# Kernel optimization log

Hardware: AMD Instinct MI355X
Metric: run time of the kernel (lower is better)

Reference implementation:

```python
import jax, jax.numpy as jnp
import numpy as np

N, T, D_MODEL, H, DK = 4, 4096, 1024, 16, 64


def setup_inputs() -> dict:
    key = jax.random.key(0)
    ks = jax.random.split(key, 16)
    randn = lambda k, sh: jax.random.normal(k, sh, dtype=jnp.float32)
    # linear weights stored (in, out) so y = x @ W + b (math-equivalent to torch Linear)
    scale = 1.0 / np.sqrt(D_MODEL)
    return {
        "x_k": randn(ks[0], (N, T, D_MODEL)),
        "x_v": randn(ks[1], (N, T, D_MODEL)),
        "x_q": randn(ks[2], (N, T, D_MODEL)),
        "mask": jnp.ones((N, T), dtype=jnp.int32),
        "Wk": randn(ks[3], (D_MODEL, H * DK)) * scale,
        "bk": randn(ks[4], (H * DK,)) * 0.02,
        "Wv": randn(ks[5], (D_MODEL, H * DK)) * scale,
        "bv": randn(ks[6], (H * DK,)) * 0.02,
        "Wq": randn(ks[7], (D_MODEL, H * DK)) * scale,
        "bq": randn(ks[8], (H * DK,)) * 0.02,
        "alpha_w": randn(ks[9], (DK,)),
        "beta_w": randn(ks[10], (DK,)),
        "Wr": randn(ks[11], (DK, DK)) * (1.0 / np.sqrt(DK)),
        "br": randn(ks[12], (DK,)) * 0.02,
        "Wfc": randn(ks[13], (H * DK, D_MODEL)) * scale,
        "bfc": randn(ks[14], (D_MODEL,)) * 0.02,
    }


def _split_heads(x):  # (n, t, h*d) -> (n, h, t, d)
    n, t, _ = x.shape
    return x.reshape(n, t, H, DK).transpose(0, 2, 1, 3)


def reference(x_k, x_v, x_q, mask, Wk, bk, Wv, bv, Wq, bq,
              alpha_w, beta_w, Wr, br, Wfc, bfc):
    scale = DK ** (-0.5)
    k = _split_heads(x_k @ Wk + bk)  # (n, h, t, d)
    v = _split_heads(x_v @ Wv + bv)
    q = _split_heads(x_q @ Wq + bq)

    m = (mask == 0)[:, None, :]  # (n, 1, t) True where masked
    neg_inf = jnp.finfo(q.dtype).min

    # alpha pooling over queries -> global query (n, h, d)
    alpha = jnp.einsum('nhtd,d->nht', q, alpha_w) * scale
    alpha = jnp.where(m, neg_inf, alpha)
    alpha = jax.nn.softmax(alpha, axis=-1)
    global_query = jnp.einsum('nht,nhtd->nhd', alpha, q)

    # p = broadcast(global_query) * k, then beta pooling -> global key
    p = global_query[:, :, None, :] * k  # (n, h, t, d)
    beta = jnp.einsum('nhtd,d->nht', p, beta_w) * scale
    beta = jnp.where(m, neg_inf, beta)
    beta = jax.nn.softmax(beta, axis=-1)
    global_key = jnp.einsum('nht,nhtd->nhd', beta, p)

    u = global_key[:, :, None, :] * v  # (n, h, t, d)
    u_r = u @ Wr + br
    A = u_r + q  # (n, h, t, d)
    A = A.transpose(0, 2, 1, 3).reshape(N, T, H * DK)
    return A @ Wfc + bfc
```

## Files before the change

### kernel.cpp

```cpp
#include <hip/hip_runtime.h>

typedef __bf16 bf16x8 __attribute__((ext_vector_type(8)));
typedef float f32x4 __attribute__((ext_vector_type(4)));
typedef unsigned int u32x4 __attribute__((ext_vector_type(4)));
typedef unsigned short u16x4 __attribute__((ext_vector_type(4)));
typedef unsigned short u16x8 __attribute__((ext_vector_type(8)));

#define SEQ_T 4096
#define DMODEL 1024
#define HEADS 16
#define DKH 64
#define MTOK 16384

#define AS1 __attribute__((address_space(1)))
#define AS3 __attribute__((address_space(3)))

__device__ __forceinline__ unsigned short f2bf(float f) {
  unsigned u = __builtin_bit_cast(unsigned int, f);
  u += 0x7FFFu + ((u >> 16) & 1u);
  return (unsigned short)(u >> 16);
}
__device__ __forceinline__ float bf2f(unsigned short h) {
  unsigned u = ((unsigned)h) << 16;
  return __builtin_bit_cast(float, u);
}
__device__ __forceinline__ void gload16(const unsigned short* g, unsigned short* l) {
  __builtin_amdgcn_global_load_lds((const AS1 unsigned int*)(g),
                                   (AS3 unsigned int*)(l), 16, 0, 0);
}

__device__ __forceinline__ void cvt_block(const float* __restrict__ x,
                                          unsigned short* __restrict__ y,
                                          size_t b, int tid) {
  f32x4 a[4];
#pragma unroll
  for (int i = 0; i < 4; ++i) a[i] = *(const f32x4*)(x + b + i * 1024 + tid * 4);
#pragma unroll
  for (int i = 0; i < 4; ++i) {
    u16x4 o;
#pragma unroll
    for (int j = 0; j < 4; ++j) o[j] = f2bf(a[i][j]);
    *(u16x4*)(y + b + i * 1024 + tid * 4) = o;
  }
}

__global__ void __launch_bounds__(256) k_cvt(const float* __restrict__ x,
                                             unsigned short* __restrict__ y) {
  cvt_block(x, y, (size_t)blockIdx.x * 4096, threadIdx.x);
}

__global__ void __launch_bounds__(256) k_cvt3(const float* __restrict__ xq,
                                              const float* __restrict__ xk,
                                              const float* __restrict__ xv,
                                              unsigned short* __restrict__ oq,
                                              unsigned short* __restrict__ ok,
                                              unsigned short* __restrict__ ov) {
  const int which = blockIdx.x >> 12;
  const float* x = which == 0 ? xq : (which == 1 ? xk : xv);
  unsigned short* y = which == 0 ? oq : (which == 1 ? ok : ov);
  cvt_block(x, y, (size_t)(blockIdx.x & 4095) * 4096, threadIdx.x);
}

__global__ void __launch_bounds__(256) k_wtrans(const float* __restrict__ W,
                                                unsigned short* __restrict__ Wt,
                                                int K, int N) {
  __shared__ float tile[32][33];
  int bn = blockIdx.x * 32, bk = blockIdx.y * 32;
  int tx = threadIdx.x, ty = threadIdx.y;
#pragma unroll
  for (int j = 0; j < 32; j += 8)
    tile[ty + j][tx] = W[(size_t)(bk + ty + j) * N + bn + tx];
  __syncthreads();
#pragma unroll
  for (int j = 0; j < 32; j += 8)
    Wt[(size_t)(bn + ty + j) * K + bk + tx] = f2bf(tile[tx][ty + j]);
}

#define BM 128
#define BN 128
#define BK 64

template <int OBF, int SCORE, int FUSEA>
__global__ void __launch_bounds__(256, 2)
k_gemm(const unsigned short* __restrict__ A, const unsigned short* __restrict__ Bt,
       const float* __restrict__ bias, void* __restrict__ C,
       const int* __restrict__ mask, const float* __restrict__ swt,
       float* __restrict__ sbuf, const unsigned short* __restrict__ qadd,
       int M, int N, int K) {
  __shared__ unsigned short As[BM * BK];
  __shared__ unsigned short Bs[BN * BK];
  const int tid = threadIdx.x;
  const int lane = tid & 63, wid = tid >> 6;
  const int wr = wid >> 1, wc = wid & 1;
  const int l15 = lane & 15, l4 = lane >> 4;

  const int nwg = gridDim.x * gridDim.y;
  const int flat = blockIdx.x + blockIdx.y * gridDim.x;
  const int rm = (flat & 7) * (nwg >> 3) + (flat >> 3);
  const int bx = rm % gridDim.x, by = rm / gridDim.x;
  const int bm = by * BM, bn = bx * BN;

  const unsigned short* Btn = FUSEA ? Bt + ((size_t)(bm >> 12) << 20) : Bt;
  const float* biasn = FUSEA ? bias + ((bm >> 12) << 10) : bias;

  f32x4 acc[4][4];
#pragma unroll
  for (int i = 0; i < 4; ++i)
#pragma unroll
    for (int j = 0; j < 4; ++j)
#pragma unroll
      for (int e = 0; e < 4; ++e) acc[i][j][e] = 0.f;

  const int sgr = lane >> 3;
  const int sgc = (lane & 7) ^ sgr;

  for (int kt = 0; kt < K; kt += BK) {
    __syncthreads();
#pragma unroll
    for (int j = 0; j < 4; ++j) {
      int rb = wid * 32 + j * 8;
      gload16(A + (size_t)(bm + rb + sgr) * K + kt + sgc * 8, As + rb * BK);
    }
#pragma unroll
    for (int j = 0; j < 4; ++j) {
      int rb = wid * 32 + j * 8;
      gload16(Btn + (size_t)(bn + rb + sgr) * K + kt + sgc * 8, Bs + rb * BK);
    }
    __syncthreads();
#pragma unroll
    for (int kh = 0; kh < 2; ++kh) {
      bf16x8 af[4], bfr[4];
#pragma unroll
      for (int m = 0; m < 4; ++m) {
        int ra = wr * 64 + m * 16 + l15;
        int sl = (kh * 4 + l4) ^ (ra & 7);
        af[m] = *(const bf16x8*)(As + ra * BK + sl * 8);
      }
#pragma unroll
      for (int n = 0; n < 4; ++n) {
        int rb = wc * 64 + n * 16 + l15;
        int sl = (kh * 4 + l4) ^ (rb & 7);
        bfr[n] = *(const bf16x8*)(Bs + rb * BK + sl * 8);
      }
#pragma unroll
      for (int m = 0; m < 4; ++m)
#pragma unroll
        for (int n = 0; n < 4; ++n)
          acc[m][n] = __builtin_amdgcn_mfma_f32_16x16x32_bf16(af[m], bfr[n],
                                                              acc[m][n], 0, 0, 0);
    }
  }

  const int crow = bm + wr * 64 + l4 * 4;
  const int ccol = bn + wc * 64 + l15;

  float pacc[4][4];
  const float* wrow = nullptr;
  if (SCORE == 1) wrow = swt;
  if (SCORE) {
#pragma unroll
    for (int m = 0; m < 4; ++m)
#pragma unroll
      for (int e = 0; e < 4; ++e) pacc[m][e] = 0.f;
  }

#pragma unroll
  for (int m = 0; m < 4; ++m)
#pragma unroll
    for (int n = 0; n < 4; ++n) {
      int c = ccol + n * 16;
      float bj = biasn[c];
      float wg = SCORE ? wrow[n * 16 + l15] : 0.f;
#pragma unroll
      for (int e = 0; e < 4; ++e) {
        int r = crow + m * 16 + e;
        float v = acc[m][n][e] + bj;
        if (FUSEA) v += bf2f(qadd[(size_t)r * N + c]);
        if (SCORE) pacc[m][e] += v * wg;
        if (OBF)
          ((unsigned short*)C)[(size_t)r * N + c] = f2bf(v);
        else
          ((float*)C)[(size_t)r * N + c] = v;
      }
    }

  if (SCORE) {
#pragma unroll
    for (int m = 0; m < 4; ++m)
#pragma unroll
      for (int e = 0; e < 4; ++e) {
        float p = pacc[m][e];
        p += __shfl_xor(p, 1);
        p += __shfl_xor(p, 2);
        p += __shfl_xor(p, 4);
        p += __shfl_xor(p, 8);
        if (l15 == 0) {
          int r = crow + m * 16 + e;
          int t = r & (SEQ_T - 1), n = r >> 12;
          float sc = p * 0.125f;
          if (mask[n * SEQ_T + t] == 0) sc = -3.0e38f;
          sbuf[((size_t)n * HEADS + bx * 2 + wc) * SEQ_T + t] = sc;
        }
      }
  }
}

__global__ void __launch_bounds__(256) k_softmax(const float* __restrict__ s,
                                                 float* __restrict__ mxo,
                                                 float* __restrict__ invo) {
  __shared__ float red[4];
  const int tid = threadIdx.x, lane = tid & 63, wid = tid >> 6;
  const float* sb = s + (size_t)blockIdx.x * SEQ_T;
  float m = -3.4e38f;
  for (int t = tid; t < SEQ_T; t += 256) m = fmaxf(m, sb[t]);
#pragma unroll
  for (int o = 1; o < 64; o <<= 1) m = fmaxf(m, __shfl_xor(m, o));
  if (lane == 0) red[wid] = m;
  __syncthreads();
  m = fmaxf(fmaxf(red[0], red[1]), fmaxf(red[2], red[3]));
  __syncthreads();
  float sum = 0.f;
  for (int t = tid; t < SEQ_T; t += 256) sum += __expf(sb[t] - m);
#pragma unroll
  for (int o = 1; o < 64; o <<= 1) sum += __shfl_xor(sum, o);
  if (lane == 0) red[wid] = sum;
  __syncthreads();
  if (tid == 0) {
    mxo[blockIdx.x] = m;
    invo[blockIdx.x] = 1.f / (red[0] + red[1] + red[2] + red[3]);
  }
}

__global__ void __launch_bounds__(256) k_wsum(const unsigned short* __restrict__ X,
                                              const float* __restrict__ s,
                                              const float* __restrict__ mxv,
                                              const float* __restrict__ invv,
                                              float* __restrict__ pbuf) {
  __shared__ float part[16][64];
  const int nh = blockIdx.x >> 4, chunk = blockIdx.x & 15;
  const int n = nh >> 4, h = nh & 15;
  const int tid = threadIdx.x, lane = tid & 63, wid = tid >> 6;
  const int tsub = lane >> 4, dl = lane & 15;
  const float mx = mxv[nh], inv = invv[nh];
  const float* sb = s + (size_t)nh * SEQ_T + chunk * 256;
  const size_t base = ((size_t)n * SEQ_T + chunk * 256) * DMODEL + h * DKH + dl * 4;
  f32x4 acc = {0.f, 0.f, 0.f, 0.f};
  for (int t = wid * 4 + tsub; t < 256; t += 16) {
    float w = __expf(sb[t] - mx) * inv;
    u16x4 xv = *(const u16x4*)(X + base + (size_t)t * DMODEL);
    acc[0] += w * bf2f(xv[0]);
    acc[1] += w * bf2f(xv[1]);
    acc[2] += w * bf2f(xv[2]);
    acc[3] += w * bf2f(xv[3]);
  }
  int g = wid * 4 + tsub;
#pragma unroll
  for (int e = 0; e < 4; ++e) part[g][dl * 4 + e] = acc[e];
  __syncthreads();
  if (tid < 64) {
    float v = 0.f;
#pragma unroll
    for (int gg = 0; gg < 16; ++gg) v += part[gg][tid];
    pbuf[(size_t)blockIdx.x * 64 + tid] = v;
  }
}

__global__ void __launch_bounds__(256) k_wksb(const float* __restrict__ Wk,
                                              const float* __restrict__ bk,
                                              const float* __restrict__ pbuf,
                                              const float* __restrict__ bw,
                                              float* __restrict__ gq,
                                              unsigned short* __restrict__ WksT,
                                              float* __restrict__ bks) {
  const int nh = blockIdx.x, tid = threadIdx.x;
  const int n = nh >> 4, h = nh & 15;
  __shared__ float wvs[64];
  if (tid < 64) {
    float v = 0.f;
#pragma unroll
    for (int c = 0; c < 16; ++c) v += pbuf[((size_t)nh * 16 + c) * 64 + tid];
    gq[(size_t)nh * 64 + tid] = v;
    wvs[tid] = v * bw[tid];
  }
  __syncthreads();
  int c0 = tid * 4;
  u16x4 o;
#pragma unroll
  for (int i = 0; i < 4; ++i) {
    int c = c0 + i;
    const float* wr = Wk + (size_t)c * DMODEL + h * DKH;
    float acc = 0.f;
#pragma unroll
    for (int dd = 0; dd < 64; dd += 4) {
      f32x4 w4 = *(const f32x4*)(wr + dd);
      acc += w4[0] * wvs[dd] + w4[1] * wvs[dd + 1] + w4[2] * wvs[dd + 2] +
             w4[3] * wvs[dd + 3];
    }
    o[i] = f2bf(acc);
  }
  *(u16x4*)(WksT + (size_t)n * 16 * DMODEL + (size_t)h * DMODEL + c0) = o;
  if (tid < 64) {
    float p = bk[h * 64 + tid] * wvs[tid];
#pragma unroll
    for (int ofs = 1; ofs < 64; ofs <<= 1) p += __shfl_xor(p, ofs);
    if (tid == 0) bks[nh] = p;
  }
}

__global__ void __launch_bounds__(128) k_score(const unsigned short* __restrict__ xk,
                                               const unsigned short* __restrict__ WksT,
                                               const float* __restrict__ bks,
                                               const int* __restrict__ mask,
                                               float* __restrict__ sbuf) {
  __shared__ unsigned short Xs[64 * 32];
  __shared__ unsigned short Ws[16 * 32];
  const int tid = threadIdx.x, lane = tid & 63, wid = tid >> 6;
  const int l15 = lane & 15, l4 = lane >> 4;
  const int bm = blockIdx.x * 64;
  const int n = bm >> 12;
  const unsigned short* Wn = WksT + (size_t)n * 16 * DMODEL;

  f32x4 acc[2];
#pragma unroll
  for (int m = 0; m < 2; ++m)
#pragma unroll
    for (int e = 0; e < 4; ++e) acc[m][e] = 0.f;

  const int srow = lane >> 2, scol = (lane & 3) * 8;
  for (int kt = 0; kt < DMODEL; kt += 32) {
    __syncthreads();
#pragma unroll
    for (int j = 0; j < 2; ++j) {
      int rb = wid * 32 + j * 16;
      gload16(xk + (size_t)(bm + rb + srow) * DMODEL + kt + scol, Xs + rb * 32);
    }
    if (wid == 0) gload16(Wn + (size_t)srow * DMODEL + kt + scol, Ws);
    __syncthreads();
    bf16x8 bfr = *(const bf16x8*)(Ws + l15 * 32 + l4 * 8);
#pragma unroll
    for (int m = 0; m < 2; ++m) {
      bf16x8 af = *(const bf16x8*)(Xs + (wid * 32 + m * 16 + l15) * 32 + l4 * 8);
      acc[m] = __builtin_amdgcn_mfma_f32_16x16x32_bf16(af, bfr, acc[m], 0, 0, 0);
    }
  }
  const int h = l15;
  const float bh = bks[n * 16 + h];
#pragma unroll
  for (int m = 0; m < 2; ++m)
#pragma unroll
    for (int e = 0; e < 4; ++e) {
      int r = bm + wid * 32 + m * 16 + l4 * 4 + e;
      int t = r & (SEQ_T - 1);
      float sc = (acc[m][e] + bh) * 0.125f;
      if (mask[n * SEQ_T + t] == 0) sc = -3.0e38f;
      sbuf[((size_t)n * HEADS + h) * SEQ_T + t] = sc;
    }
}

__global__ void __launch_bounds__(256) k_bwsum(const unsigned short* __restrict__ xk,
                                               const float* __restrict__ s,
                                               const float* __restrict__ smx,
                                               const float* __restrict__ sinv,
                                               float* __restrict__ part) {
  __shared__ float eb[16][64];
  const int tc = blockIdx.x, n = blockIdx.y, tid = threadIdx.x;
#pragma unroll
  for (int i = 0; i < 4; ++i) {
    int idx = i * 256 + tid;
    int h = idx >> 6, t = idx & 63;
    int nh = n * 16 + h;
    eb[h][t] = __expf(s[(size_t)nh * SEQ_T + tc * 64 + t] - smx[nh]) * sinv[nh];
  }
  __syncthreads();
  const int c0 = tid * 4;
  f32x4 acc[16];
#pragma unroll
  for (int h = 0; h < 16; ++h)
#pragma unroll
    for (int e = 0; e < 4; ++e) acc[h][e] = 0.f;
  const unsigned short* xb = xk + ((size_t)n * SEQ_T + tc * 64) * DMODEL + c0;
  for (int t = 0; t < 64; ++t) {
    u16x4 xr = *(const u16x4*)(xb + (size_t)t * DMODEL);
    float x0 = bf2f(xr[0]), x1 = bf2f(xr[1]), x2 = bf2f(xr[2]), x3 = bf2f(xr[3]);
#pragma unroll
    for (int h = 0; h < 16; ++h) {
      float w = eb[h][t];
      acc[h][0] += w * x0;
      acc[h][1] += w * x1;
      acc[h][2] += w * x2;
      acc[h][3] += w * x3;
    }
  }
#pragma unroll
  for (int h = 0; h < 16; ++h)
    *(f32x4*)(part + (((size_t)(n * 64 + tc)) * 16 + h) * DMODEL + c0) = acc[h];
}

__global__ void __launch_bounds__(256) k_gkrw(const float* __restrict__ part,
                                              const unsigned short* __restrict__ WkT,
                                              const float* __restrict__ bk,
                                              const float* __restrict__ gq,
                                              const float* __restrict__ Wr,
                                              const float* __restrict__ bv,
                                              const float* __restrict__ br,
                                              unsigned short* __restrict__ WrgT,
                                              float* __restrict__ bcomb) {
  __shared__ float pl[DMODEL];
  __shared__ float gks[64];
  __shared__ float wl[4096];
  const int nh = blockIdx.x, tid = threadIdx.x;
  const int n = nh >> 4, h = nh & 15;
  const int c0 = tid * 4;
  f32x4 a4 = {0.f, 0.f, 0.f, 0.f};
  for (int tc = 0; tc < 64; ++tc) {
    f32x4 p = *(const f32x4*)(part + (((size_t)(n * 64 + tc)) * 16 + h) * DMODEL + c0);
    a4[0] += p[0]; a4[1] += p[1]; a4[2] += p[2]; a4[3] += p[3];
  }
#pragma unroll
  for (int e = 0; e < 4; ++e) pl[c0 + e] = a4[e];
  __syncthreads();
  if (tid < 64) {
    const unsigned short* wr = WkT + (size_t)(h * 64 + tid) * DMODEL;
    float acc = 0.f;
    for (int c = 0; c < DMODEL; c += 8) {
      u16x8 w = *(const u16x8*)(wr + c);
#pragma unroll
      for (int j = 0; j < 8; ++j) acc += pl[c + j] * bf2f(w[j]);
    }
    gks[tid] = gq[(size_t)nh * 64 + tid] * (acc + bk[h * 64 + tid]);
  }
  __syncthreads();
#pragma unroll
  for (int i = 0; i < 16; ++i) {
    int idx = i * 256 + tid;
    int d = idx >> 6, dd = idx & 63;
    float v = gks[dd] * Wr[dd * 64 + d];
    wl[idx] = v;
    WrgT[(size_t)nh * 4096 + idx] = f2bf(v);
  }
  __syncthreads();
  if (tid < 64) {
    float acc = br[tid];
#pragma unroll
    for (int dd = 0; dd < 64; ++dd) acc += bv[h * 64 + dd] * wl[tid * 64 + dd];
    bcomb[(size_t)n * DMODEL + h * 64 + tid] = acc;
  }
}

#define LDW 72
__global__ void __launch_bounds__(256) k_wcomb(const unsigned short* __restrict__ WrgT,
                                               const unsigned short* __restrict__ WvN,
                                               unsigned short* __restrict__ WcombT) {
  __shared__ unsigned short Wg[64 * LDW];
  __shared__ unsigned short Vv[128 * LDW];
  const int rc = blockIdx.x, nh = blockIdx.y;
  const int n = nh >> 4, h = nh & 15;
  const int tid = threadIdx.x, lane = tid & 63, wid = tid >> 6;
  const int l15 = lane & 15, l4 = lane >> 4;
#pragma unroll
  for (int i = 0; i < 2; ++i) {
    int v = i * 256 + tid;
    int d = v >> 3, k8 = v & 7;
    *(u16x8*)(Wg + d * LDW + k8 * 8) =
        *(const u16x8*)(WrgT + (size_t)nh * 4096 + d * 64 + k8 * 8);
  }
#pragma unroll
  for (int i = 0; i < 4; ++i) {
    int v = i * 256 + tid;
    int r = v >> 3, k8 = v & 7;
    *(u16x8*)(Vv + r * LDW + k8 * 8) =
        *(const u16x8*)(WvN + (size_t)(rc * 128 + r) * DMODEL + h * 64 + k8 * 8);
  }
  __syncthreads();
  f32x4 acc[8];
#pragma unroll
  for (int ct = 0; ct < 8; ++ct)
#pragma unroll
    for (int e = 0; e < 4; ++e) acc[ct][e] = 0.f;
#pragma unroll
  for (int ks = 0; ks < 2; ++ks) {
    bf16x8 af = *(const bf16x8*)(Wg + (wid * 16 + l15) * LDW + ks * 32 + l4 * 8);
#pragma unroll
    for (int ct = 0; ct < 8; ++ct) {
      bf16x8 bf = *(const bf16x8*)(Vv + (ct * 16 + l15) * LDW + ks * 32 + l4 * 8);
      acc[ct] = __builtin_amdgcn_mfma_f32_16x16x32_bf16(af, bf, acc[ct], 0, 0, 0);
    }
  }
  unsigned short* out = WcombT + ((size_t)n << 20);
#pragma unroll
  for (int ct = 0; ct < 8; ++ct)
#pragma unroll
    for (int e = 0; e < 4; ++e) {
      int d = h * 64 + wid * 16 + l4 * 4 + e;
      int r = rc * 128 + ct * 16 + l15;
      out[(size_t)d * DMODEL + r] = f2bf(acc[ct][e]);
    }
}

extern "C" void kernel_launch(void* const* d_in, const int* in_sizes, int n_in,
                              void* d_out, int out_size, void* d_ws, size_t ws_size,
                              hipStream_t stream) {
  const float* x_k = (const float*)d_in[0];
  const float* x_v = (const float*)d_in[1];
  const float* x_q = (const float*)d_in[2];
  const int* mask = (const int*)d_in[3];
  const float* Wk = (const float*)d_in[4];
  const float* bk = (const float*)d_in[5];
  const float* Wv = (const float*)d_in[6];
  const float* bv = (const float*)d_in[7];
  const float* Wq = (const float*)d_in[8];
  const float* bq = (const float*)d_in[9];
  const float* alpha_w = (const float*)d_in[10];
  const float* beta_w = (const float*)d_in[11];
  const float* Wr = (const float*)d_in[12];
  const float* br = (const float*)d_in[13];
  const float* Wfc = (const float*)d_in[14];
  const float* bfc = (const float*)d_in[15];

  unsigned short* qbf = (unsigned short*)d_out;
  unsigned short* xvb = (unsigned short*)d_out + (size_t)MTOK * DMODEL;

  char* ws = (char*)d_ws;
  const size_t MB = 1024 * 1024;
  unsigned short* xst = (unsigned short*)(ws);
  unsigned short* abuf = (unsigned short*)(ws + 32 * MB);
  unsigned short* WqT = (unsigned short*)(ws + 64 * MB);
  unsigned short* WkT = WqT + (size_t)DMODEL * DMODEL;
  unsigned short* WfT = WkT + (size_t)DMODEL * DMODEL;
  unsigned short* WvN = WfT + (size_t)DMODEL * DMODEL;
  unsigned short* WcombT = WvN + (size_t)DMODEL * DMODEL;
  unsigned short* WrgT = WcombT + (size_t)4 * DMODEL * DMODEL;
  unsigned short* WksT = WrgT + (size_t)64 * 4096;
  float* part = (float*)(WksT + (size_t)4 * 16 * DMODEL);
  float* sbuf = part + (size_t)256 * 16 * DMODEL;
  float* pbuf = sbuf + (size_t)64 * SEQ_T;
  float* smx = pbuf + 1024 * 64;
  float* sinv = smx + 64;
  float* gq = sinv + 64;
  float* bks = gq + 4096;
  float* bcomb = bks + 64;

  dim3 tb(32, 8);
  dim3 tg(DMODEL / 32, DMODEL / 32);
  k_wtrans<<<tg, tb, 0, stream>>>(Wq, WqT, DMODEL, DMODEL);
  k_wtrans<<<tg, tb, 0, stream>>>(Wk, WkT, DMODEL, DMODEL);
  k_wtrans<<<tg, tb, 0, stream>>>(Wfc, WfT, DMODEL, DMODEL);
  k_cvt<<<256, 256, 0, stream>>>(Wv, WvN);

  k_cvt3<<<3 * 4096, 256, 0, stream>>>(x_q, x_k, x_v, xst, abuf, xvb);

  dim3 ggrid(DMODEL / BN, MTOK / BM);

  k_gemm<1, 1, 0><<<ggrid, 256, 0, stream>>>(xst, WqT, bq, (void*)qbf, mask,
                                             alpha_w, sbuf, nullptr,
                                             MTOK, DMODEL, DMODEL);
  k_softmax<<<64, 256, 0, stream>>>(sbuf, smx, sinv);
  k_wsum<<<1024, 256, 0, stream>>>(qbf, sbuf, smx, sinv, pbuf);
  k_wksb<<<64, 256, 0, stream>>>(Wk, bk, pbuf, beta_w, gq, WksT, bks);

  k_score<<<MTOK / 64, 128, 0, stream>>>(abuf, WksT, bks, mask, sbuf);
  k_softmax<<<64, 256, 0, stream>>>(sbuf, smx, sinv);
  dim3 bwg(64, 4);
  k_bwsum<<<bwg, 256, 0, stream>>>(abuf, sbuf, smx, sinv, part);
  k_gkrw<<<64, 256, 0, stream>>>(part, WkT, bk, gq, Wr, bv, br, WrgT, bcomb);

  dim3 wcg(8, 64);
  k_wcomb<<<wcg, 256, 0, stream>>>(WrgT, WvN, WcombT);

  k_gemm<1, 0, 1><<<ggrid, 256, 0, stream>>>(xvb, WcombT, bcomb, (void*)abuf,
                                             nullptr, nullptr, nullptr, qbf,
                                             MTOK, DMODEL, DMODEL);

  k_gemm<0, 0, 0><<<ggrid, 256, 0, stream>>>(abuf, WfT, bfc, d_out, nullptr,
                                             nullptr, nullptr, nullptr,
                                             MTOK, DMODEL, DMODEL);
}
```

Measured before the change: 277.0 us.

## Overlap x_k/x_v bf16 conversion with Q-projection GEMM via interleaved blocks

After: 282.9 us. 2.1% more time.

```diff
diff --git a/kernel.cpp b/kernel.cpp
--- a/kernel.cpp
+++ b/kernel.cpp
@@ -47,18 +47,6 @@
 __global__ void __launch_bounds__(256) k_cvt(const float* __restrict__ x,
                                              unsigned short* __restrict__ y) {
   cvt_block(x, y, (size_t)blockIdx.x * 4096, threadIdx.x);
-}
-
-__global__ void __launch_bounds__(256) k_cvt3(const float* __restrict__ xq,
-                                              const float* __restrict__ xk,
-                                              const float* __restrict__ xv,
-                                              unsigned short* __restrict__ oq,
-                                              unsigned short* __restrict__ ok,
-                                              unsigned short* __restrict__ ov) {
-  const int which = blockIdx.x >> 12;
-  const float* x = which == 0 ? xq : (which == 1 ? xk : xv);
-  unsigned short* y = which == 0 ? oq : (which == 1 ? ok : ov);
-  cvt_block(x, y, (size_t)(blockIdx.x & 4095) * 4096, threadIdx.x);
 }
 
 __global__ void __launch_bounds__(256) k_wtrans(const float* __restrict__ W,
@@ -80,24 +68,44 @@
 #define BN 128
 #define BK 64
 
-template <int OBF, int SCORE, int FUSEA>
+template <int OBF, int SCORE, int FUSEA, int CVT>
 __global__ void __launch_bounds__(256, 2)
 k_gemm(const unsigned short* __restrict__ A, const unsigned short* __restrict__ Bt,
        const float* __restrict__ bias, void* __restrict__ C,
        const int* __restrict__ mask, const float* __restrict__ swt,
        float* __restrict__ sbuf, const unsigned short* __restrict__ qadd,
+       const float* __restrict__ cvx0, const float* __restrict__ cvx1,
+       unsigned short* __restrict__ cvy0, unsigned short* __restrict__ cvy1,
        int M, int N, int K) {
   __shared__ unsigned short As[BM * BK];
   __shared__ unsigned short Bs[BN * BK];
   const int tid = threadIdx.x;
+
+  int flat;
+  if (CVT) {
+    const int grp = blockIdx.x >> 4, sub = blockIdx.x & 15;
+    if (sub >= 8) {
+      int j = grp * 8 + (sub - 8);
+      const float* x = (j < 512) ? cvx0 : cvx1;
+      unsigned short* y = (j < 512) ? cvy0 : cvy1;
+      size_t base = (size_t)(j & 511) * 32768;
+#pragma unroll
+      for (int c = 0; c < 8; ++c) cvt_block(x, y, base + c * 4096, tid);
+      return;
+    }
+    flat = grp * 8 + sub;
+  } else {
+    flat = blockIdx.x;
+  }
+
   const int lane = tid & 63, wid = tid >> 6;
   const int wr = wid >> 1, wc = wid & 1;
   const int l15 = lane & 15, l4 = lane >> 4;
 
-  const int nwg = gridDim.x * gridDim.y;
-  const int flat = blockIdx.x + blockIdx.y * gridDim.x;
+  const int gx = N / BN;
+  const int nwg = gx * (M / BM);
   const int rm = (flat & 7) * (nwg >> 3) + (flat >> 3);
-  const int bx = rm % gridDim.x, by = rm / gridDim.x;
+  const int bx = rm % gx, by = rm / gx;
   const int bm = by * BM, bn = bx * BN;
 
   const unsigned short* Btn = FUSEA ? Bt + ((size_t)(bm >> 12) << 20) : Bt;
@@ -547,13 +555,12 @@
   k_wtrans<<<tg, tb, 0, stream>>>(Wfc, WfT, DMODEL, DMODEL);
   k_cvt<<<256, 256, 0, stream>>>(Wv, WvN);
 
-  k_cvt3<<<3 * 4096, 256, 0, stream>>>(x_q, x_k, x_v, xst, abuf, xvb);
-
-  dim3 ggrid(DMODEL / BN, MTOK / BM);
-
-  k_gemm<1, 1, 0><<<ggrid, 256, 0, stream>>>(xst, WqT, bq, (void*)qbf, mask,
-                                             alpha_w, sbuf, nullptr,
-                                             MTOK, DMODEL, DMODEL);
+  k_cvt<<<4096, 256, 0, stream>>>(x_q, xst);
+
+  k_gemm<1, 1, 0, 1><<<2048, 256, 0, stream>>>(xst, WqT, bq, (void*)qbf, mask,
+                                               alpha_w, sbuf, nullptr,
+                                               x_k, x_v, abuf, xvb,
+                                               MTOK, DMODEL, DMODEL);
   k_softmax<<<64, 256, 0, stream>>>(sbuf, smx, sinv);
   k_wsum<<<1024, 256, 0, stream>>>(qbf, sbuf, smx, sinv, pbuf);
   k_wksb<<<64, 256, 0, stream>>>(Wk, bk, pbuf, beta_w, gq, WksT, bks);
@@ -567,11 +574,13 @@
   dim3 wcg(8, 64);
   k_wcomb<<<wcg, 256, 0, stream>>>(WrgT, WvN, WcombT);
 
-  k_gemm<1, 0, 1><<<ggrid, 256, 0, stream>>>(xvb, WcombT, bcomb, (void*)abuf,
-                                             nullptr, nullptr, nullptr, qbf,
-                                             MTOK, DMODEL, DMODEL);
-
-  k_gemm<0, 0, 0><<<ggrid, 256, 0, stream>>>(abuf, WfT, bfc, d_out, nullptr,
-                                             nullptr, nullptr, nullptr,
-                                             MTOK, DMODEL, DMODEL);
-}
+  k_gemm<1, 0, 1, 0><<<1024, 256, 0, stream>>>(xvb, WcombT, bcomb, (void*)abuf,
+                                               nullptr, nullptr, nullptr, qbf,
+                                               nullptr, nullptr, nullptr, nullptr,
+                                               MTOK, DMODEL, DMODEL);
+
+  k_gemm<0, 0, 0, 0><<<1024, 256, 0, stream>>>(abuf, WfT, bfc, d_out, nullptr,
+                                               nullptr, nullptr, nullptr,
+                                               nullptr, nullptr, nullptr, nullptr,
+                                               MTOK, DMODEL, DMODEL);
+}
```
